# Kernel optimization log

Measured on AMD Instinct MI355X. Metric: run time of the kernel, lower is better.

Reference implementation:

```python
import jax, jax.numpy as jnp
import numpy as np

NUM_HEADS = 12
T_TASK = 0  # current task index (training uses prompts[:, t:t+1])


def setup_inputs() -> dict:
    key = jax.random.key(0)
    ks = jax.random.split(key, 6)
    B, N, C = 64, 197, 768
    G = 8            # num_selectors
    P = 8            # num_prompts
    NT = 10          # num_tasks
    hd = C // NUM_HEADS
    return {
        "x": jax.random.normal(ks[0], (B, N, C), dtype=jnp.float32),
        "tokens": jax.random.normal(ks[1], (1, B, 1 + G, C), dtype=jnp.float32),
        "qkv_w": jax.random.normal(ks[2], (3 * C, C), dtype=jnp.float32) * 0.02,
        "proj_w": jax.random.normal(ks[3], (C, C), dtype=jnp.float32) * 0.02,
        "proj_b": jax.random.normal(ks[4], (C,), dtype=jnp.float32) * 0.02,
        "prompts": jax.random.normal(ks[5], (2, NT, P, NUM_HEADS, hd), dtype=jnp.float32),
    }


def _forward(x, tokens, qkv_w, proj_w, proj_b, prompts):
    C = x.shape[-1]
    hd = C // NUM_HEADS
    scale = hd ** -0.5
    token_scale = C ** -0.5

    # ---- selector cross-attention (x detached) ----
    xd = jax.lax.stop_gradient(x)
    task_cls = tokens[:, :, 0:1]        # [T,B,1,C]
    selectors = tokens[:, :, 1:]        # [T,B,G,C]
    g_attn = jnp.einsum('tbsc,bnc->tbsn', selectors, xd) * token_scale
    g_soft = jax.nn.softmax(g_attn, axis=-1)
    task_patches = jnp.einsum('bnc,tbsn->tbsc', xd, g_soft)
    task_x = jnp.concatenate([task_cls, task_patches], axis=2)  # [T,B,H,C]
    T, B, H, _ = task_x.shape

    # ---- prompt-augmented task attention ----
    qkv = (task_x @ qkv_w.T).reshape(T, B, H, 3, NUM_HEADS, hd)
    qkv = qkv.transpose(3, 0, 1, 4, 2, 5)          # [3,T,B,heads,H,hd]
    q, k, v = qkv[0], qkv[1], qkv[2]

    pr = prompts[:, T_TASK:T_TASK + 1]             # [2,1,P,heads,hd] (training slice)
    P = pr.shape[2]
    pr = jnp.broadcast_to(pr[:, :, None], (2, 1, B, P, NUM_HEADS, hd))
    pr = pr.transpose(0, 1, 2, 4, 3, 5)            # [2,1,B,heads,P,hd]
    k = jnp.concatenate([pr[0], k], axis=-2)       # [T,B,heads,P+H,hd]
    v = jnp.concatenate([pr[1], v], axis=-2)

    attn = jax.nn.softmax((q @ jnp.swapaxes(k, -2, -1)) * scale, axis=-1)
    out = jnp.swapaxes(attn @ v, 2, 3).reshape(T, B, H, C)
    task_out = out @ proj_w.T + proj_b

    # disable_dandr == False, tome == 0 -> keep selectors, replace cls
    tokens_out = jnp.concatenate([task_out[:, :, 0:1], selectors], axis=2)

    # ---- frozen standard patch attention (no_grad) ----
    Bn, N, _ = x.shape
    qkv2 = (xd @ qkv_w.T).reshape(Bn, N, 3, NUM_HEADS, hd).transpose(2, 0, 3, 1, 4)
    q2, k2, v2 = qkv2[0], qkv2[1], qkv2[2]
    a2 = jax.nn.softmax((q2 @ jnp.swapaxes(k2, -2, -1)) * scale, axis=-1)
    xo = jnp.swapaxes(a2 @ v2, 1, 2).reshape(Bn, N, C)
    xo = jax.lax.stop_gradient(xo @ proj_w.T + proj_b)
    return xo, tokens_out


def reference(x, tokens, qkv_w, proj_w, proj_b, prompts):
    return _forward(x, tokens, qkv_w, proj_w, proj_b, prompts)
```

## Files before the change

kernel.cpp:

```cpp
#include <hip/hip_runtime.h>
#include <hip/hip_bf16.h>
#include <cstddef>


typedef __attribute__((ext_vector_type(8))) short    bf16x8;
typedef __attribute__((ext_vector_type(8))) unsigned short ushort8;
typedef __attribute__((ext_vector_type(4))) unsigned short ushort4v;
typedef __attribute__((ext_vector_type(4))) float    f32x4;

__device__ __forceinline__ unsigned short f2bf_rne(float f) {
    unsigned int u = __float_as_uint(f);
    u += 0x7fff + ((u >> 16) & 1);
    return (unsigned short)(u >> 16);
}
__device__ __forceinline__ float bf2f(unsigned short h) {
    return __uint_as_float(((unsigned int)h) << 16);
}

#define LDK 40

__global__ __launch_bounds__(256)
void gemm_mfma_kernel(const float* __restrict__ A, const float* __restrict__ Bw,
                      const float* __restrict__ bias, float* __restrict__ C,
                      int M, int N, int K)
{
    __shared__ unsigned short Ah[128][LDK], Al[128][LDK];
    __shared__ unsigned short Bh[128][LDK], Bl[128][LDK];

    const int tid = threadIdx.x;
    const int m0 = blockIdx.y * 128;
    const int n0 = blockIdx.x * 128;
    const int wave = tid >> 6, lane = tid & 63;
    const int wr = wave >> 1, wc = wave & 1;
    const int l15 = lane & 15, kg = lane >> 4;

    f32x4 zero4 = {0.f, 0.f, 0.f, 0.f};
    f32x4 acc[4][4];
#pragma unroll
    for (int i = 0; i < 4; ++i)
#pragma unroll
        for (int j = 0; j < 4; ++j) acc[i][j] = zero4;

    const int srow  = tid >> 1;
    const int shalf = tid & 1;
    const int sgm   = m0 + srow;
    const bool arow_ok = (sgm < M);
    const float* aptr = A  + (size_t)sgm * K + shalf * 16;
    const float* bptr = Bw + (size_t)(n0 + srow) * K + shalf * 16;

    for (int k0 = 0; k0 < K; k0 += 32) {
        f32x4 av[4], bv[4];
#pragma unroll
        for (int i = 0; i < 4; ++i) {
            av[i] = arow_ok ? *(const f32x4*)(aptr + k0 + i * 4) : zero4;
            bv[i] = *(const f32x4*)(bptr + k0 + i * 4);
        }
        __syncthreads();

        ushort8 h, l;
#pragma unroll
        for (int half = 0; half < 2; ++half) {
#pragma unroll
            for (int i = 0; i < 8; ++i) {
                float v = av[half * 2 + (i >> 2)][i & 3];
                unsigned short hh = f2bf_rne(v);
                h[i] = hh;
                l[i] = f2bf_rne(v - bf2f(hh));
            }
            *(ushort8*)&Ah[srow][shalf * 16 + half * 8] = h;
            *(ushort8*)&Al[srow][shalf * 16 + half * 8] = l;
        }
#pragma unroll
        for (int half = 0; half < 2; ++half) {
#pragma unroll
            for (int i = 0; i < 8; ++i) {
                float v = bv[half * 2 + (i >> 2)][i & 3];
                unsigned short hh = f2bf_rne(v);
                h[i] = hh;
                l[i] = f2bf_rne(v - bf2f(hh));
            }
            *(ushort8*)&Bh[srow][shalf * 16 + half * 8] = h;
            *(ushort8*)&Bl[srow][shalf * 16 + half * 8] = l;
        }
        __syncthreads();

        bf16x8 afh[4], afl[4], bfh[4], bfl[4];
#pragma unroll
        for (int f = 0; f < 4; ++f) {
            const int ar = wr * 64 + f * 16 + l15;
            afh[f] = *(const bf16x8*)&Ah[ar][kg * 8];
            afl[f] = *(const bf16x8*)&Al[ar][kg * 8];
            const int br = wc * 64 + f * 16 + l15;
            bfh[f] = *(const bf16x8*)&Bh[br][kg * 8];
            bfl[f] = *(const bf16x8*)&Bl[br][kg * 8];
        }
#pragma unroll
        for (int fm = 0; fm < 4; ++fm)
#pragma unroll
            for (int fn = 0; fn < 4; ++fn) {
                acc[fm][fn] = __builtin_amdgcn_mfma_f32_16x16x32_bf16(
                    afh[fm], bfh[fn], acc[fm][fn], 0, 0, 0);
                acc[fm][fn] = __builtin_amdgcn_mfma_f32_16x16x32_bf16(
                    afh[fm], bfl[fn], acc[fm][fn], 0, 0, 0);
                acc[fm][fn] = __builtin_amdgcn_mfma_f32_16x16x32_bf16(
                    afl[fm], bfh[fn], acc[fm][fn], 0, 0, 0);
            }
    }

#pragma unroll
    for (int fm = 0; fm < 4; ++fm)
#pragma unroll
        for (int fn = 0; fn < 4; ++fn) {
            const int col = n0 + wc * 64 + fn * 16 + l15;
            const float bvv = bias ? bias[col] : 0.f;
#pragma unroll
            for (int j = 0; j < 4; ++j) {
                const int row = m0 + wr * 64 + fm * 16 + kg * 4 + j;
                if (row < M) C[(size_t)row * N + col] = acc[fm][fn][j] + bvv;
            }
        }
}

__global__ __launch_bounds__(256)
void task_gather_kernel(const float* __restrict__ x, const float* __restrict__ tokens,
                        float* __restrict__ task_x, float* __restrict__ out_tok)
{
    const int b = blockIdx.x;
    const int tid = threadIdx.x;
    __shared__ float sel[8][772];
    __shared__ float g[8][200];

    for (int l = tid; l < 8 * 192; l += 256) {
        int s = l / 192, c4 = l % 192;
        float4 v = *(const float4*)&tokens[((size_t)b * 9 + 1 + s) * 768 + c4 * 4];
        sel[s][c4 * 4 + 0] = v.x; sel[s][c4 * 4 + 1] = v.y;
        sel[s][c4 * 4 + 2] = v.z; sel[s][c4 * 4 + 3] = v.w;
        *(float4*)&out_tok[((size_t)b * 9 + 1 + s) * 768 + c4 * 4] = v;
    }
    __syncthreads();

    const float token_scale = 0.03608439182435161f;
    for (int idx = tid; idx < 197 * 8; idx += 256) {
        int n = idx >> 3, s = idx & 7;
        const float* xr = &x[((size_t)b * 197 + n) * 768];
        float acc = 0.f;
        for (int c4 = 0; c4 < 192; ++c4) {
            float4 xv = *(const float4*)&xr[c4 * 4];
            acc = fmaf(xv.x, sel[s][c4 * 4 + 0], acc);
            acc = fmaf(xv.y, sel[s][c4 * 4 + 1], acc);
            acc = fmaf(xv.z, sel[s][c4 * 4 + 2], acc);
            acc = fmaf(xv.w, sel[s][c4 * 4 + 3], acc);
        }
        g[s][n] = acc * token_scale;
    }
    __syncthreads();

    const int w = tid >> 6, lane = tid & 63;
    for (int s = w; s < 8; s += 4) {
        float vals[4];
        float m = -1e30f;
#pragma unroll
        for (int t = 0; t < 4; ++t) {
            int n = lane + 64 * t;
            vals[t] = (n < 197) ? g[s][n] : -1e30f;
            m = fmaxf(m, vals[t]);
        }
#pragma unroll
        for (int off = 32; off >= 1; off >>= 1) m = fmaxf(m, __shfl_xor(m, off, 64));
        float sum = 0.f;
#pragma unroll
        for (int t = 0; t < 4; ++t) {
            int n = lane + 64 * t;
            if (n < 197) { vals[t] = __expf(vals[t] - m); sum += vals[t]; }
        }
#pragma unroll
        for (int off = 32; off >= 1; off >>= 1) sum += __shfl_xor(sum, off, 64);
        float inv = 1.f / sum;
#pragma unroll
        for (int t = 0; t < 4; ++t) {
            int n = lane + 64 * t;
            if (n < 197) g[s][n] = vals[t] * inv;
        }
    }
    __syncthreads();

    if (tid < 192) {
        float4 acc8[8];
#pragma unroll
        for (int s = 0; s < 8; ++s) acc8[s] = make_float4(0.f, 0.f, 0.f, 0.f);
        for (int n = 0; n < 197; ++n) {
            float4 xv = *(const float4*)&x[((size_t)b * 197 + n) * 768 + tid * 4];
#pragma unroll
            for (int s = 0; s < 8; ++s) {
                float gw = g[s][n];
                acc8[s].x = fmaf(gw, xv.x, acc8[s].x);
                acc8[s].y = fmaf(gw, xv.y, acc8[s].y);
                acc8[s].z = fmaf(gw, xv.z, acc8[s].z);
                acc8[s].w = fmaf(gw, xv.w, acc8[s].w);
            }
        }
#pragma unroll
        for (int s = 0; s < 8; ++s)
            *(float4*)&task_x[((size_t)b * 9 + 1 + s) * 768 + tid * 4] = acc8[s];
        float4 cls = *(const float4*)&tokens[((size_t)b * 9) * 768 + tid * 4];
        *(float4*)&task_x[((size_t)b * 9) * 768 + tid * 4] = cls;
    }
}

__global__ __launch_bounds__(256)
void attn_mfma_kernel(const float* __restrict__ qkv2, float* __restrict__ attn_o)
{
    __shared__ alignas(16) unsigned short Khi[198][64], Klo[198][64];
    __shared__ alignas(16) unsigned short Vthi[64][232], Vtlo[64][232];
    __shared__ alignas(16) unsigned short Phi[4][16][208], Plo[4][16][208];

    const int h = blockIdx.x, b = blockIdx.y;
    const int tid = threadIdx.x;
    const int wave = tid >> 6, lane = tid & 63;
    const int l15 = lane & 15, kg = lane >> 4;

    const size_t base = (size_t)b * 197 * 2304 + (size_t)h * 64;

    for (int l = tid; l < 197 * 16; l += 256) {
        int n = l >> 4, d4 = l & 15;
        const float* p = &qkv2[base + (size_t)n * 2304 + d4 * 4];
        float4 k4 = *(const float4*)(p + 768);
        float4 v4 = *(const float4*)(p + 1536);
        float kf[4] = {k4.x, k4.y, k4.z, k4.w};
        float vf[4] = {v4.x, v4.y, v4.z, v4.w};
        const int off = (((d4 >> 1) ^ (n & 7)) << 3) + ((d4 & 1) << 2);
        ushort4v kh, kl;
#pragma unroll
        for (int i = 0; i < 4; ++i) {
            unsigned short hh = f2bf_rne(kf[i]);
            kh[i] = hh;
            kl[i] = f2bf_rne(kf[i] - bf2f(hh));
        }
        *(ushort4v*)&Khi[n][off] = kh;
        *(ushort4v*)&Klo[n][off] = kl;
#pragma unroll
        for (int i = 0; i < 4; ++i) {
            unsigned short hh = f2bf_rne(vf[i]);
            Vthi[d4 * 4 + i][n] = hh;
            Vtlo[d4 * 4 + i][n] = f2bf_rne(vf[i] - bf2f(hh));
        }
    }
    for (int l = tid; l < 64 * 11; l += 256) {
        int d = l / 11, c = 197 + l % 11;
        Vthi[d][c] = 0;
        Vtlo[d][c] = 0;
    }
    __syncthreads();

    for (int qt = wave; qt < 13; qt += 4) {
        const int n0 = qt * 16;
        const int qrow = (n0 + l15 < 197) ? (n0 + l15) : 196;

        bf16x8 qh[2], ql[2];
#pragma unroll
        for (int s = 0; s < 2; ++s) {
            const float* qp = &qkv2[base + (size_t)qrow * 2304 + kg * 8 + 32 * s];
            float4 qa = *(const float4*)qp;
            float4 qb = *(const float4*)(qp + 4);
            float qf[8] = {qa.x, qa.y, qa.z, qa.w, qb.x, qb.y, qb.z, qb.w};
#pragma unroll
            for (int i = 0; i < 8; ++i) {
                float v = qf[i] * 0.125f;
                unsigned short hh = f2bf_rne(v);
                qh[s][i] = (short)hh;
                ql[s][i] = (short)f2bf_rne(v - bf2f(hh));
            }
        }

        f32x4 st[13];
#pragma unroll
        for (int t = 0; t < 13; ++t) st[t] = (f32x4){0.f, 0.f, 0.f, 0.f};
#pragma unroll
        for (int t = 0; t < 13; ++t) {
            const int r = 16 * t + l15;
            const bool ok = (t < 12) || (l15 < 5);
#pragma unroll
            for (int s = 0; s < 2; ++s) {
                bf16x8 kh = {0, 0, 0, 0, 0, 0, 0, 0};
                bf16x8 kl = {0, 0, 0, 0, 0, 0, 0, 0};
                if (ok) {
                    const int off = (((kg + 4 * s) ^ (l15 & 7)) << 3);
                    kh = *(const bf16x8*)&Khi[r][off];
                    kl = *(const bf16x8*)&Klo[r][off];
                }
                st[t] = __builtin_amdgcn_mfma_f32_16x16x32_bf16(kh, qh[s], st[t], 0, 0, 0);
                st[t] = __builtin_amdgcn_mfma_f32_16x16x32_bf16(kh, ql[s], st[t], 0, 0, 0);
                st[t] = __builtin_amdgcn_mfma_f32_16x16x32_bf16(kl, qh[s], st[t], 0, 0, 0);
            }
        }

        float m = -1e30f;
#pragma unroll
        for (int t = 0; t < 13; ++t)
#pragma unroll
            for (int j = 0; j < 4; ++j) {
                const int key = 16 * t + kg * 4 + j;
                float v = (key < 197) ? st[t][j] : -1e30f;
                st[t][j] = v;
                m = fmaxf(m, v);
            }
        m = fmaxf(m, __shfl_xor(m, 16, 64));
        m = fmaxf(m, __shfl_xor(m, 32, 64));
        float sum = 0.f;
#pragma unroll
        for (int t = 0; t < 13; ++t)
#pragma unroll
            for (int j = 0; j < 4; ++j) {
                float e = __expf(st[t][j] - m);
                st[t][j] = e;
                sum += e;
            }
        sum += __shfl_xor(sum, 16, 64);
        sum += __shfl_xor(sum, 32, 64);
        const float inv = 1.f / sum;

#pragma unroll
        for (int t = 0; t < 13; ++t) {
            ushort4v ph, pl;
#pragma unroll
            for (int j = 0; j < 4; ++j) {
                unsigned short hh = f2bf_rne(st[t][j]);
                ph[j] = hh;
                pl[j] = f2bf_rne(st[t][j] - bf2f(hh));
            }
            *(ushort4v*)&Phi[wave][l15][16 * t + kg * 4] = ph;
            *(ushort4v*)&Plo[wave][l15][16 * t + kg * 4] = pl;
        }

        f32x4 ao[4];
#pragma unroll
        for (int fd = 0; fd < 4; ++fd) ao[fd] = (f32x4){0.f, 0.f, 0.f, 0.f};
#pragma unroll
        for (int s = 0; s < 7; ++s) {
            const bool act = (s < 6) || (kg < 2);
            bf16x8 ph = {0, 0, 0, 0, 0, 0, 0, 0};
            bf16x8 pl = {0, 0, 0, 0, 0, 0, 0, 0};
            if (act) {
                ph = *(const bf16x8*)&Phi[wave][l15][kg * 8 + 32 * s];
                pl = *(const bf16x8*)&Plo[wave][l15][kg * 8 + 32 * s];
            }
#pragma unroll
            for (int fd = 0; fd < 4; ++fd) {
                bf16x8 vh = {0, 0, 0, 0, 0, 0, 0, 0};
                bf16x8 vl = {0, 0, 0, 0, 0, 0, 0, 0};
                if (act) {
                    vh = *(const bf16x8*)&Vthi[fd * 16 + l15][kg * 8 + 32 * s];
                    vl = *(const bf16x8*)&Vtlo[fd * 16 + l15][kg * 8 + 32 * s];
                }
                ao[fd] = __builtin_amdgcn_mfma_f32_16x16x32_bf16(vh, ph, ao[fd], 0, 0, 0);
                ao[fd] = __builtin_amdgcn_mfma_f32_16x16x32_bf16(vh, pl, ao[fd], 0, 0, 0);
                ao[fd] = __builtin_amdgcn_mfma_f32_16x16x32_bf16(vl, ph, ao[fd], 0, 0, 0);
            }
        }

        if (n0 + l15 < 197) {
            float* op = &attn_o[((size_t)(b * 197 + n0 + l15)) * 768 + h * 64];
#pragma unroll
            for (int fd = 0; fd < 4; ++fd) {
                float4 o = make_float4(ao[fd][0] * inv, ao[fd][1] * inv,
                                       ao[fd][2] * inv, ao[fd][3] * inv);
                *(float4*)(op + fd * 16 + kg * 4) = o;
            }
        }
    }
}

__global__ __launch_bounds__(64)
void task_attn2_kernel(const float* __restrict__ task_qkv, const float* __restrict__ prompts,
                       float* __restrict__ out0)
{
    const int h = blockIdx.x, b = blockIdx.y;
    const int d = threadIdx.x;

    const float q0 = task_qkv[((size_t)b * 9) * 2304 + h * 64 + d] * 0.125f;

    float s[17];
#pragma unroll
    for (int j = 0; j < 17; ++j) {
        float kv = (j < 8)
            ? prompts[(size_t)(j * 12 + h) * 64 + d]
            : task_qkv[((size_t)b * 9 + (j - 8)) * 2304 + 768 + h * 64 + d];
        float prod = q0 * kv;
#pragma unroll
        for (int off = 32; off >= 1; off >>= 1) prod += __shfl_xor(prod, off, 64);
        s[j] = prod;
    }
    float m = s[0];
#pragma unroll
    for (int j = 1; j < 17; ++j) m = fmaxf(m, s[j]);
    float sum = 0.f;
#pragma unroll
    for (int j = 0; j < 17; ++j) { s[j] = __expf(s[j] - m); sum += s[j]; }
    float acc = 0.f;
#pragma unroll
    for (int j = 0; j < 17; ++j) {
        float vv = (j < 8)
            ? prompts[(size_t)61440 + (size_t)(j * 12 + h) * 64 + d]
            : task_qkv[((size_t)b * 9 + (j - 8)) * 2304 + 1536 + h * 64 + d];
        acc = fmaf(s[j], vv, acc);
    }
    out0[((size_t)b * 12 + h) * 64 + d] = acc / sum;
}

__global__ __launch_bounds__(256)
void task_proj_kernel(const float* __restrict__ out0, const float* __restrict__ proj_w,
                      const float* __restrict__ proj_b, float* __restrict__ out_tok)
{
    const int b = blockIdx.x;
    const int col = blockIdx.y * 256 + threadIdx.x;
    __shared__ float xr[768];
    for (int l = threadIdx.x; l < 768; l += 256) xr[l] = out0[(size_t)b * 768 + l];
    __syncthreads();
    const float* wp = &proj_w[(size_t)col * 768];
    float acc = proj_b[col];
    for (int c4 = 0; c4 < 192; ++c4) {
        float4 wv = *(const float4*)&wp[c4 * 4];
        acc = fmaf(wv.x, xr[c4 * 4 + 0], acc);
        acc = fmaf(wv.y, xr[c4 * 4 + 1], acc);
        acc = fmaf(wv.z, xr[c4 * 4 + 2], acc);
        acc = fmaf(wv.w, xr[c4 * 4 + 3], acc);
    }
    out_tok[((size_t)b * 9) * 768 + col] = acc;
}

extern "C" void kernel_launch(void* const* d_in, const int* in_sizes, int n_in,
                              void* d_out, int out_size, void* d_ws, size_t ws_size,
                              hipStream_t stream)
{
    const float* x       = (const float*)d_in[0];
    const float* tokens  = (const float*)d_in[1];
    const float* qkv_w   = (const float*)d_in[2];
    const float* proj_w  = (const float*)d_in[3];
    const float* proj_b  = (const float*)d_in[4];
    const float* prompts = (const float*)d_in[5];

    float* xo      = (float*)d_out;
    float* out_tok = xo + (size_t)12608 * 768;

    float* qkv2     = (float*)d_ws;
    float* attn_o   = qkv2 + (size_t)12608 * 2304;
    float* task_x   = attn_o + (size_t)12608 * 768;
    float* out0     = task_x + (size_t)64 * 9 * 768;
    float* task_qkv = out0 + (size_t)64 * 768;

    task_gather_kernel<<<dim3(64), 256, 0, stream>>>(x, tokens, task_x, out_tok);

    gemm_mfma_kernel<<<dim3(2304 / 128, (12608 + 127) / 128), 256, 0, stream>>>(
        x, qkv_w, nullptr, qkv2, 12608, 2304, 768);

    attn_mfma_kernel<<<dim3(12, 64), 256, 0, stream>>>(qkv2, attn_o);

    gemm_mfma_kernel<<<dim3(768 / 128, (12608 + 127) / 128), 256, 0, stream>>>(
        attn_o, proj_w, proj_b, xo, 12608, 768, 768);

    gemm_mfma_kernel<<<dim3(2304 / 128, (576 + 127) / 128), 256, 0, stream>>>(
        task_x, qkv_w, nullptr, task_qkv, 576, 2304, 768);

    task_attn2_kernel<<<dim3(12, 64), 64, 0, stream>>>(task_qkv, prompts, out0);

    task_proj_kernel<<<dim3(64, 3), 256, 0, stream>>>(out0, proj_w, proj_b, out_tok);
}
```

Measured before the change: 698.7 us.

## Pre-split operands into bf16 hi/lo arrays before the GEMM kernels

```diff
diff --git a/kernel.cpp b/kernel.cpp
--- a/kernel.cpp
+++ b/kernel.cpp
@@ -1,6 +1,7 @@
 #include <hip/hip_runtime.h>
 #include <hip/hip_bf16.h>
 #include <cstddef>
+#include <cstdint>
 
 
 typedef __attribute__((ext_vector_type(8))) short    bf16x8;
@@ -17,15 +18,35 @@
     return __uint_as_float(((unsigned int)h) << 16);
 }
 
-#define LDK 40
-
 __global__ __launch_bounds__(256)
-void gemm_mfma_kernel(const float* __restrict__ A, const float* __restrict__ Bw,
-                      const float* __restrict__ bias, float* __restrict__ C,
-                      int M, int N, int K)
-{
-    __shared__ unsigned short Ah[128][LDK], Al[128][LDK];
-    __shared__ unsigned short Bh[128][LDK], Bl[128][LDK];
+void split_hl_kernel(const float* __restrict__ in, unsigned short* __restrict__ hi,
+                     unsigned short* __restrict__ lo, int n4)
+{
+    int i = blockIdx.x * 256 + threadIdx.x;
+    const int stride = gridDim.x * 256;
+    for (; i < n4; i += stride) {
+        float4 v = ((const float4*)in)[i];
+        float f[4] = {v.x, v.y, v.z, v.w};
+        ushort4v h4, l4;
+#pragma unroll
+        for (int j = 0; j < 4; ++j) {
+            unsigned short hh = f2bf_rne(f[j]);
+            h4[j] = hh;
+            l4[j] = f2bf_rne(f[j] - bf2f(hh));
+        }
+        ((ushort4v*)hi)[i] = h4;
+        ((ushort4v*)lo)[i] = l4;
+    }
+}
+
+__global__ __launch_bounds__(256)
+void gemm_hl_kernel(const unsigned short* __restrict__ Ah_g, const unsigned short* __restrict__ Al_g,
+                    const unsigned short* __restrict__ Bh_g, const unsigned short* __restrict__ Bl_g,
+                    const float* __restrict__ bias, float* __restrict__ C,
+                    int M, int N, int K)
+{
+    __shared__ alignas(16) unsigned short As_h[128][32], As_l[128][32];
+    __shared__ alignas(16) unsigned short Bs_h[128][32], Bs_l[128][32];
 
     const int tid = threadIdx.x;
     const int m0 = blockIdx.y * 128;
@@ -34,65 +55,52 @@
     const int wr = wave >> 1, wc = wave & 1;
     const int l15 = lane & 15, kg = lane >> 4;
 
-    f32x4 zero4 = {0.f, 0.f, 0.f, 0.f};
     f32x4 acc[4][4];
 #pragma unroll
     for (int i = 0; i < 4; ++i)
 #pragma unroll
-        for (int j = 0; j < 4; ++j) acc[i][j] = zero4;
-
-    const int srow  = tid >> 1;
-    const int shalf = tid & 1;
-    const int sgm   = m0 + srow;
-    const bool arow_ok = (sgm < M);
-    const float* aptr = A  + (size_t)sgm * K + shalf * 16;
-    const float* bptr = Bw + (size_t)(n0 + srow) * K + shalf * 16;
+        for (int j = 0; j < 4; ++j) acc[i][j] = (f32x4){0.f, 0.f, 0.f, 0.f};
+
+    const unsigned short* srcbase =
+        (wave == 0) ? Ah_g : (wave == 1) ? Al_g : (wave == 2) ? Bh_g : Bl_g;
+    unsigned short* ldsbase =
+        (wave == 0) ? &As_h[0][0] : (wave == 1) ? &As_l[0][0]
+                                  : (wave == 2) ? &Bs_h[0][0] : &Bs_l[0][0];
+    const bool isA = (wave < 2);
+    const int rbase = isA ? m0 : n0;
+    const int rmax  = isA ? (M - 1) : (N - 1);
+
+    const unsigned short* sp[8];
+#pragma unroll
+    for (int c = 0; c < 8; ++c) {
+        int r = rbase + c * 16 + (lane >> 2);
+        if (r > rmax) r = rmax;
+        sp[c] = srcbase + (size_t)r * K + (lane & 3) * 8;
+    }
+    const int loff = (lane >> 2) * 32 + (lane & 3) * 8;
 
     for (int k0 = 0; k0 < K; k0 += 32) {
-        f32x4 av[4], bv[4];
-#pragma unroll
-        for (int i = 0; i < 4; ++i) {
-            av[i] = arow_ok ? *(const f32x4*)(aptr + k0 + i * 4) : zero4;
-            bv[i] = *(const f32x4*)(bptr + k0 + i * 4);
+        ushort8 stg[8];
+#pragma unroll
+        for (int c = 0; c < 8; ++c) {
+            stg[c] = *(const ushort8*)sp[c];
+            sp[c] += 32;
         }
         __syncthreads();
-
-        ushort8 h, l;
-#pragma unroll
-        for (int half = 0; half < 2; ++half) {
-#pragma unroll
-            for (int i = 0; i < 8; ++i) {
-                float v = av[half * 2 + (i >> 2)][i & 3];
-                unsigned short hh = f2bf_rne(v);
-                h[i] = hh;
-                l[i] = f2bf_rne(v - bf2f(hh));
-            }
-            *(ushort8*)&Ah[srow][shalf * 16 + half * 8] = h;
-            *(ushort8*)&Al[srow][shalf * 16 + half * 8] = l;
-        }
-#pragma unroll
-        for (int half = 0; half < 2; ++half) {
-#pragma unroll
-            for (int i = 0; i < 8; ++i) {
-                float v = bv[half * 2 + (i >> 2)][i & 3];
-                unsigned short hh = f2bf_rne(v);
-                h[i] = hh;
-                l[i] = f2bf_rne(v - bf2f(hh));
-            }
-            *(ushort8*)&Bh[srow][shalf * 16 + half * 8] = h;
-            *(ushort8*)&Bl[srow][shalf * 16 + half * 8] = l;
-        }
+#pragma unroll
+        for (int c = 0; c < 8; ++c)
+            *(ushort8*)(ldsbase + c * 512 + loff) = stg[c];
         __syncthreads();
 
         bf16x8 afh[4], afl[4], bfh[4], bfl[4];
 #pragma unroll
         for (int f = 0; f < 4; ++f) {
             const int ar = wr * 64 + f * 16 + l15;
-            afh[f] = *(const bf16x8*)&Ah[ar][kg * 8];
-            afl[f] = *(const bf16x8*)&Al[ar][kg * 8];
+            afh[f] = *(const bf16x8*)&As_h[ar][kg * 8];
+            afl[f] = *(const bf16x8*)&As_l[ar][kg * 8];
             const int br = wc * 64 + f * 16 + l15;
-            bfh[f] = *(const bf16x8*)&Bh[br][kg * 8];
-            bfl[f] = *(const bf16x8*)&Bl[br][kg * 8];
+            bfh[f] = *(const bf16x8*)&Bs_h[br][kg * 8];
+            bfl[f] = *(const bf16x8*)&Bs_l[br][kg * 8];
         }
 #pragma unroll
         for (int fm = 0; fm < 4; ++fm)
@@ -123,7 +131,8 @@
 
 __global__ __launch_bounds__(256)
 void task_gather_kernel(const float* __restrict__ x, const float* __restrict__ tokens,
-                        float* __restrict__ task_x, float* __restrict__ out_tok)
+                        unsigned short* __restrict__ tx_hi, unsigned short* __restrict__ tx_lo,
+                        float* __restrict__ out_tok)
 {
     const int b = blockIdx.x;
     const int tid = threadIdx.x;
@@ -200,15 +209,35 @@
             }
         }
 #pragma unroll
-        for (int s = 0; s < 8; ++s)
-            *(float4*)&task_x[((size_t)b * 9 + 1 + s) * 768 + tid * 4] = acc8[s];
+        for (int s = 0; s < 8; ++s) {
+            float f[4] = {acc8[s].x, acc8[s].y, acc8[s].z, acc8[s].w};
+            ushort4v h4, l4;
+#pragma unroll
+            for (int j = 0; j < 4; ++j) {
+                unsigned short hh = f2bf_rne(f[j]);
+                h4[j] = hh;
+                l4[j] = f2bf_rne(f[j] - bf2f(hh));
+            }
+            *(ushort4v*)&tx_hi[((size_t)b * 9 + 1 + s) * 768 + tid * 4] = h4;
+            *(ushort4v*)&tx_lo[((size_t)b * 9 + 1 + s) * 768 + tid * 4] = l4;
+        }
         float4 cls = *(const float4*)&tokens[((size_t)b * 9) * 768 + tid * 4];
-        *(float4*)&task_x[((size_t)b * 9) * 768 + tid * 4] = cls;
+        float cf[4] = {cls.x, cls.y, cls.z, cls.w};
+        ushort4v h4, l4;
+#pragma unroll
+        for (int j = 0; j < 4; ++j) {
+            unsigned short hh = f2bf_rne(cf[j]);
+            h4[j] = hh;
+            l4[j] = f2bf_rne(cf[j] - bf2f(hh));
+        }
+        *(ushort4v*)&tx_hi[((size_t)b * 9) * 768 + tid * 4] = h4;
+        *(ushort4v*)&tx_lo[((size_t)b * 9) * 768 + tid * 4] = l4;
     }
 }
 
 __global__ __launch_bounds__(256)
-void attn_mfma_kernel(const float* __restrict__ qkv2, float* __restrict__ attn_o)
+void attn_mfma_kernel(const float* __restrict__ qkv2,
+                      unsigned short* __restrict__ ao_hi, unsigned short* __restrict__ ao_lo)
 {
     __shared__ alignas(16) unsigned short Khi[198][64], Klo[198][64];
     __shared__ alignas(16) unsigned short Vthi[64][232], Vtlo[64][232];
@@ -359,12 +388,19 @@
         }
 
         if (n0 + l15 < 197) {
-            float* op = &attn_o[((size_t)(b * 197 + n0 + l15)) * 768 + h * 64];
+            const size_t ob = ((size_t)(b * 197 + n0 + l15)) * 768 + h * 64;
 #pragma unroll
             for (int fd = 0; fd < 4; ++fd) {
-                float4 o = make_float4(ao[fd][0] * inv, ao[fd][1] * inv,
-                                       ao[fd][2] * inv, ao[fd][3] * inv);
-                *(float4*)(op + fd * 16 + kg * 4) = o;
+                ushort4v h4, l4;
+#pragma unroll
+                for (int j = 0; j < 4; ++j) {
+                    float v = ao[fd][j] * inv;
+                    unsigned short hh = f2bf_rne(v);
+                    h4[j] = hh;
+                    l4[j] = f2bf_rne(v - bf2f(hh));
+                }
+                *(ushort4v*)&ao_hi[ob + fd * 16 + kg * 4] = h4;
+                *(ushort4v*)&ao_lo[ob + fd * 16 + kg * 4] = l4;
             }
         }
     }
@@ -442,24 +478,36 @@
     float* xo      = (float*)d_out;
     float* out_tok = xo + (size_t)12608 * 768;
 
-    float* qkv2     = (float*)d_ws;
-    float* attn_o   = qkv2 + (size_t)12608 * 2304;
-    float* task_x   = attn_o + (size_t)12608 * 768;
-    float* out0     = task_x + (size_t)64 * 9 * 768;
-    float* task_qkv = out0 + (size_t)64 * 768;
-
-    task_gather_kernel<<<dim3(64), 256, 0, stream>>>(x, tokens, task_x, out_tok);
-
-    gemm_mfma_kernel<<<dim3(2304 / 128, (12608 + 127) / 128), 256, 0, stream>>>(
-        x, qkv_w, nullptr, qkv2, 12608, 2304, 768);
-
-    attn_mfma_kernel<<<dim3(12, 64), 256, 0, stream>>>(qkv2, attn_o);
-
-    gemm_mfma_kernel<<<dim3(768 / 128, (12608 + 127) / 128), 256, 0, stream>>>(
-        attn_o, proj_w, proj_b, xo, 12608, 768, 768);
-
-    gemm_mfma_kernel<<<dim3(2304 / 128, (576 + 127) / 128), 256, 0, stream>>>(
-        task_x, qkv_w, nullptr, task_qkv, 576, 2304, 768);
+    float*          qkv2  = (float*)d_ws;
+    unsigned short* x_hi  = (unsigned short*)(qkv2 + (size_t)29048832);
+    unsigned short* x_lo  = x_hi + (size_t)9682944;
+    unsigned short* ao_hi = x_hi;
+    unsigned short* ao_lo = x_lo;
+    unsigned short* w_hi  = x_lo + (size_t)9682944;
+    unsigned short* w_lo  = w_hi + (size_t)1769472;
+    unsigned short* pw_hi = w_lo + (size_t)1769472;
+    unsigned short* pw_lo = pw_hi + (size_t)589824;
+    unsigned short* tx_hi = pw_lo + (size_t)589824;
+    unsigned short* tx_lo = tx_hi + (size_t)442368;
+    float* task_qkv = (float*)(tx_lo + (size_t)442368);
+    float* out0     = task_qkv + (size_t)1327104;
+
+    split_hl_kernel<<<2048, 256, 0, stream>>>(x, x_hi, x_lo, 12608 * 768 / 4);
+    split_hl_kernel<<<1728, 256, 0, stream>>>(qkv_w, w_hi, w_lo, 2304 * 768 / 4);
+    split_hl_kernel<<<576, 256, 0, stream>>>(proj_w, pw_hi, pw_lo, 768 * 768 / 4);
+
+    task_gather_kernel<<<dim3(64), 256, 0, stream>>>(x, tokens, tx_hi, tx_lo, out_tok);
+
+    gemm_hl_kernel<<<dim3(2304 / 128, (12608 + 127) / 128), 256, 0, stream>>>(
+        x_hi, x_lo, w_hi, w_lo, nullptr, qkv2, 12608, 2304, 768);
+
+    attn_mfma_kernel<<<dim3(12, 64), 256, 0, stream>>>(qkv2, ao_hi, ao_lo);
+
+    gemm_hl_kernel<<<dim3(768 / 128, (12608 + 127) / 128), 256, 0, stream>>>(
+        ao_hi, ao_lo, pw_hi, pw_lo, proj_b, xo, 12608, 768, 768);
+
+    gemm_hl_kernel<<<dim3(2304 / 128, (576 + 127) / 128), 256, 0, stream>>>(
+        tx_hi, tx_lo, w_hi, w_lo, nullptr, task_qkv, 576, 2304, 768);
 
     task_attn2_kernel<<<dim3(12, 64), 64, 0, stream>>>(task_qkv, prompts, out0);
 
```

Result: faster. 623.7 us (-10.7%).
